# Kernel tuning notes

Hardware: AMD Instinct MI355X
Metric: run time of the kernel (lower is better)

The kernel has to match this reference:

```python
import jax, jax.numpy as jnp
import numpy as np

BLOCK = 16
NUM_HEADS = 12
EMBED = 768
LN_EPS = 1e-6


def setup_inputs() -> dict:
    key = jax.random.key(0)
    ks = jax.random.split(key, 6)
    H = W = 1024
    x = jax.random.normal(ks[0], (H, W), dtype=jnp.float32)
    # Conv2d(1, EMBED, kernel=BLOCK, stride=BLOCK) weights, flattened to [E, b*b]
    proj_w = jax.random.normal(ks[1], (EMBED, BLOCK * BLOCK), dtype=jnp.float32) * 0.02
    proj_b = jax.random.normal(ks[2], (EMBED,), dtype=jnp.float32) * 0.02
    ln_g = jnp.ones((EMBED,), dtype=jnp.float32)
    ln_b = jnp.zeros((EMBED,), dtype=jnp.float32)
    # nn.Linear(E, 3E, bias=False): weight [3E, E]
    qkv_w = jax.random.normal(ks[3], (3 * EMBED, EMBED), dtype=jnp.float32) * 0.02
    return {"x": x, "proj_w": proj_w, "proj_b": proj_b,
            "ln_g": ln_g, "ln_b": ln_b, "qkv_w": qkv_w}


def reference(x, proj_w, proj_b, ln_g, ln_b, qkv_w):
    H, W = x.shape
    b = BLOCK
    # Patch embed: conv with kernel=stride=b on a single-channel image is
    # exactly patchify + matmul. Token order matches flatten(2) (row-major).
    patches = x.reshape(H // b, b, W // b, b).transpose(0, 2, 1, 3)
    patches = patches.reshape((H // b) * (W // b), b * b)      # [N, b*b]
    tok = patches @ proj_w.T + proj_b                          # [N, E]

    # LayerNorm (eps=1e-6)
    mu = jnp.mean(tok, axis=-1, keepdims=True)
    var = jnp.mean(jnp.square(tok - mu), axis=-1, keepdims=True)
    tok = (tok - mu) * jax.lax.rsqrt(var + LN_EPS) * ln_g + ln_b

    # Attention (batch = 1)
    N, C = tok.shape
    h, d = NUM_HEADS, C // NUM_HEADS
    qkv = (tok @ qkv_w.T).reshape(N, 3, h, d)                  # [N, 3, h, d]
    q = qkv[:, 0].transpose(1, 0, 2)                            # [h, N, d]
    k = qkv[:, 1].transpose(1, 0, 2)
    v = qkv[:, 2].transpose(1, 0, 2)
    scale = d ** -0.5
    attn = jax.nn.softmax(jnp.einsum('hnd,hmd->hnm', q, k) * scale, axis=-1)
    out = jnp.einsum('hnm,hmd->hnd', attn, v)                   # [h, N, d]
    out = out.transpose(1, 0, 2).reshape(N, C)                  # [N, C]
    return out[None]                                            # [1, N, C]
```

## Files before the change

kernel.cpp:

```cpp
#include <hip/hip_runtime.h>
#include <hip/hip_bf16.h>

typedef __bf16 bf16_t;
typedef __attribute__((ext_vector_type(8))) __bf16 bf16x8;
typedef __attribute__((ext_vector_type(4))) __bf16 bf16x4;
typedef __attribute__((ext_vector_type(4))) float f32x4;
typedef __attribute__((ext_vector_type(4))) unsigned int uint4v;

#define QSCALE 0.1803368801111204f

static __device__ inline void glds16(const bf16_t* g, bf16_t* l) {
    __builtin_amdgcn_global_load_lds(
        (__attribute__((address_space(1))) const void*)g,
        (__attribute__((address_space(3))) void*)l,
        16, 0, 0);
}

static __device__ inline float hwexp2(float x) {
#if __has_builtin(__builtin_amdgcn_exp2f)
    return __builtin_amdgcn_exp2f(x);
#else
    float r;
    asm("v_exp_f32 %0, %1" : "=v"(r) : "v"(x));
    return r;
#endif
}

static __device__ inline unsigned int pack_trunc(float lo, float hi) {
    return __builtin_amdgcn_perm(__builtin_bit_cast(unsigned int, hi),
                                 __builtin_bit_cast(unsigned int, lo),
                                 0x07060302u);
}

__global__ void cvt2_kernel(const float* __restrict__ a, bf16_t* __restrict__ oa, int na4,
                            const float* __restrict__ b, bf16_t* __restrict__ ob, int nb4) {
    int i = blockIdx.x * 256 + threadIdx.x;
    if (i < na4) {
        float4 v = ((const float4*)a)[i];
        bf16x4 o = {(bf16_t)v.x, (bf16_t)v.y, (bf16_t)v.z, (bf16_t)v.w};
        ((bf16x4*)oa)[i] = o;
    } else {
        int j = i - na4;
        if (j < nb4) {
            float4 v = ((const float4*)b)[j];
            bf16x4 o = {(bf16_t)v.x, (bf16_t)v.y, (bf16_t)v.z, (bf16_t)v.w};
            ((bf16x4*)ob)[j] = o;
        }
    }
}

__global__ __launch_bounds__(256) void patch_gemm(const float* __restrict__ x,
                                                  const bf16_t* __restrict__ pw,
                                                  const float* __restrict__ pb,
                                                  float* __restrict__ tok) {
    const int bm = blockIdx.x;
    const int bn = blockIdx.y;
    const int tid = threadIdx.x;

    __shared__ bf16_t At[64][264];
    __shared__ bf16_t Bt[64][264];

    #pragma unroll
    for (int t = 0; t < 16; t++) {
        int linear = tid + t * 256;
        int ml = linear >> 6;
        int kv = (linear & 63) << 2;
        int n = bm * 64 + ml;
        int pr = n >> 6, pc = n & 63;
        int i = kv >> 4, j = kv & 15;
        float4 v = *(const float4*)(x + (pr * 16 + i) * 1024 + pc * 16 + j);
        bf16x4 o = {(bf16_t)v.x, (bf16_t)v.y, (bf16_t)v.z, (bf16_t)v.w};
        *(bf16x4*)(&At[ml][kv]) = o;
    }
    #pragma unroll
    for (int t = 0; t < 8; t++) {
        int linear = tid + t * 256;
        int nl = linear >> 5;
        int kv = (linear & 31) << 3;
        *(int4*)(&Bt[nl][kv]) = *(const int4*)(pw + (size_t)(bn * 64 + nl) * 256 + kv);
    }
    __syncthreads();

    const int lane = tid & 63, wid = tid >> 6, ln = lane & 15, quad = lane >> 4;
    f32x4 acc[4];
    #pragma unroll
    for (int s = 0; s < 4; s++) acc[s] = {0.f, 0.f, 0.f, 0.f};

    #pragma unroll
    for (int kk = 0; kk < 8; kk++) {
        bf16x8 af = *(const bf16x8*)(&At[wid * 16 + ln][kk * 32 + quad * 8]);
        #pragma unroll
        for (int s = 0; s < 4; s++) {
            bf16x8 bfr = *(const bf16x8*)(&Bt[s * 16 + ln][kk * 32 + quad * 8]);
            acc[s] = __builtin_amdgcn_mfma_f32_16x16x32_bf16(af, bfr, acc[s], 0, 0, 0);
        }
    }

    #pragma unroll
    for (int s = 0; s < 4; s++) {
        int e = bn * 64 + s * 16 + ln;
        float bias = pb[e];
        #pragma unroll
        for (int r = 0; r < 4; r++) {
            int m = bm * 64 + wid * 16 + quad * 4 + r;
            tok[(size_t)m * 768 + e] = acc[s][r] + bias;
        }
    }
}

__global__ __launch_bounds__(256) void ln_kernel(const float* __restrict__ tok,
                                                 const float* __restrict__ g,
                                                 const float* __restrict__ b,
                                                 bf16_t* __restrict__ out) {
    const int n = blockIdx.x;
    const int tid = threadIdx.x;
    const float* row = tok + (size_t)n * 768;
    float x0 = row[tid], x1 = row[tid + 256], x2 = row[tid + 512];
    float s = x0 + x1 + x2;
    float s2 = x0 * x0 + x1 * x1 + x2 * x2;
    #pragma unroll
    for (int off = 32; off; off >>= 1) {
        s += __shfl_xor(s, off);
        s2 += __shfl_xor(s2, off);
    }
    __shared__ float ws1[4], ws2[4];
    int wid = tid >> 6;
    if ((tid & 63) == 0) { ws1[wid] = s; ws2[wid] = s2; }
    __syncthreads();
    s = ws1[0] + ws1[1] + ws1[2] + ws1[3];
    s2 = ws2[0] + ws2[1] + ws2[2] + ws2[3];
    float mu = s * (1.f / 768.f);
    float var = s2 * (1.f / 768.f) - mu * mu;
    float r = rsqrtf(var + 1e-6f);
    bf16_t* orow = out + (size_t)n * 768;
    orow[tid]       = (bf16_t)((x0 - mu) * r * g[tid]       + b[tid]);
    orow[tid + 256] = (bf16_t)((x1 - mu) * r * g[tid + 256] + b[tid + 256]);
    orow[tid + 512] = (bf16_t)((x2 - mu) * r * g[tid + 512] + b[tid + 512]);
}

__global__ __launch_bounds__(256) void qkv_gemm(const bf16_t* __restrict__ tokb,
                                                const bf16_t* __restrict__ wq,
                                                bf16_t* __restrict__ qb,
                                                bf16_t* __restrict__ kswz,
                                                bf16_t* __restrict__ vswz) {
    const int bm = blockIdx.x;
    const int bn = blockIdx.y;
    const int tid = threadIdx.x;
    const int wid = tid >> 6, lane = tid & 63;
    const int ln = lane & 15, quad = lane >> 4;
    const int wm = wid & 1, wn = wid >> 1;

    __shared__ bf16_t At[128 * 64];
    __shared__ bf16_t Bt[128 * 64];

    f32x4 acc[4][4];
    #pragma unroll
    for (int sm = 0; sm < 4; sm++)
        #pragma unroll
        for (int sn = 0; sn < 4; sn++) acc[sm][sn] = {0.f, 0.f, 0.f, 0.f};

    const int srow = wid * 32 + (lane >> 3);
    const int scol = (lane & 7) * 8;

    for (int kb0 = 0; kb0 < 768; kb0 += 64) {
        __syncthreads();
        #pragma unroll
        for (int i = 0; i < 4; i++) {
            glds16(tokb + (size_t)(bm * 128 + srow + i * 8) * 768 + kb0 + scol,
                   At + wid * 2048 + i * 512);
            glds16(wq + (size_t)(bn * 128 + srow + i * 8) * 768 + kb0 + scol,
                   Bt + wid * 2048 + i * 512);
        }
        __syncthreads();
        #pragma unroll
        for (int kk = 0; kk < 2; kk++) {
            bf16x8 af[4], bfr[4];
            #pragma unroll
            for (int s = 0; s < 4; s++) {
                af[s]  = *(const bf16x8*)(At + (wm * 64 + s * 16 + ln) * 64 + kk * 32 + quad * 8);
                bfr[s] = *(const bf16x8*)(Bt + (wn * 64 + s * 16 + ln) * 64 + kk * 32 + quad * 8);
            }
            #pragma unroll
            for (int sm = 0; sm < 4; sm++)
                #pragma unroll
                for (int sn = 0; sn < 4; sn++)
                    acc[sm][sn] = __builtin_amdgcn_mfma_f32_16x16x32_bf16(af[sm], bfr[sn], acc[sm][sn], 0, 0, 0);
        }
    }

    const int sidx = bn / 6;
    const int head = (bn % 6) * 2 + wn;
    #pragma unroll
    for (int sn = 0; sn < 4; sn++) {
        int dc = sn * 16 + ln;
        #pragma unroll
        for (int sm = 0; sm < 4; sm++) {
            #pragma unroll
            for (int r = 0; r < 4; r++) {
                int m = bm * 128 + wm * 64 + sm * 16 + quad * 4 + r;
                float v = acc[sm][sn][r];
                if (sidx == 0) {
                    qb[((size_t)(head * 4096 + m)) * 64 + dc] = (bf16_t)(v * QSCALE);
                } else if (sidx == 1) {
                    bf16_t val = (bf16_t)v;
                    int kt = m >> 6, sb = (m >> 4) & 3, lnk = m & 15;
                    int half = dc >> 5, quadk = (dc >> 3) & 3, j = dc & 7;
                    int l = quadk * 16 + lnk;
                    kswz[((size_t)(head * 64 + kt)) * 4096 + sb * 1024 + half * 512 + l * 8 + j] = val;
                } else {
                    bf16_t val = (bf16_t)v;
                    int kt = m >> 6, keyl = m & 63;
                    int sblk = keyl >> 4;
                    int mm = sblk >> 1, tb = sblk & 1;
                    int w16 = keyl & 15, qv = w16 >> 2, jj = w16 & 3;
                    int jp = tb * 4 + jj;
                    int db = dc >> 4, lnv = dc & 15;
                    int l = qv * 16 + lnv;
                    vswz[((size_t)(head * 64 + kt)) * 4096 + ((mm * 4 + db) * 64 + l) * 8 + jp] = val;
                }
            }
        }
    }
}

__global__ __launch_bounds__(256, 2) void attn_partial(const bf16_t* __restrict__ qbuf,
                                                       const bf16_t* __restrict__ kswz,
                                                       const bf16_t* __restrict__ vswz,
                                                       float* __restrict__ raw0,
                                                       float* __restrict__ raw1,
                                                       float* __restrict__ l_part) {
    const int h = blockIdx.y;
    const int chunk = blockIdx.z;
    const int tid = threadIdx.x;
    const int wid = tid >> 6;
    const int lane = tid & 63;
    const int ln = lane & 15, quad = lane >> 4;
    const int q0 = blockIdx.x * 128;

    __shared__ bf16_t Kf[2][4096];
    __shared__ bf16_t Vf[2][4096];

    bf16x8 qf[2][2];
    #pragma unroll
    for (int g = 0; g < 2; g++) {
        const int q0g = q0 + wid * 32 + g * 16;
        const bf16_t* qrow = qbuf + ((size_t)h * 4096 + q0g + ln) * 64;
        qf[g][0] = *(const bf16x8*)(qrow + quad * 8);
        qf[g][1] = *(const bf16x8*)(qrow + 32 + quad * 8);
    }

    bf16x8 ones;
    #pragma unroll
    for (int i = 0; i < 8; i++) ones[i] = (bf16_t)1.0f;

    const bf16_t* kg = kswz + (size_t)h * 64 * 4096 + (size_t)chunk * 32 * 4096;
    const bf16_t* vg = vswz + (size_t)h * 64 * 4096 + (size_t)chunk * 32 * 4096;

    f32x4 accO[2][4];
    f32x4 accL[2];
    #pragma unroll
    for (int g = 0; g < 2; g++) {
        accL[g] = {0.f, 0.f, 0.f, 0.f};
        #pragma unroll
        for (int d = 0; d < 4; d++) accO[g][d] = {0.f, 0.f, 0.f, 0.f};
    }

    auto stage = [&](int tile, int buf) {
        const bf16_t* kt_g = kg + (size_t)tile * 4096;
        const bf16_t* vt_g = vg + (size_t)tile * 4096;
        #pragma unroll
        for (int i = 0; i < 2; i++) {
            glds16(kt_g + wid * 1024 + i * 512 + lane * 8, &Kf[buf][wid * 1024 + i * 512]);
            glds16(vt_g + wid * 1024 + i * 512 + lane * 8, &Vf[buf][wid * 1024 + i * 512]);
        }
    };

    auto compute = [&](const bf16_t* Kb, const bf16_t* Vb) {
        #pragma unroll
        for (int m = 0; m < 2; m++) {
            bf16x8 vf[4];
            #pragma unroll
            for (int db = 0; db < 4; db++)
                vf[db] = *(const bf16x8*)(Vb + m * 2048 + db * 512 + lane * 8);
            bf16x8 kfa0 = *(const bf16x8*)(Kb + (2 * m) * 1024 + lane * 8);
            bf16x8 kfa1 = *(const bf16x8*)(Kb + (2 * m) * 1024 + 512 + lane * 8);
            bf16x8 kfb0 = *(const bf16x8*)(Kb + (2 * m + 1) * 1024 + lane * 8);
            bf16x8 kfb1 = *(const bf16x8*)(Kb + (2 * m + 1) * 1024 + 512 + lane * 8);
            #pragma unroll
            for (int g = 0; g < 2; g++) {
                f32x4 z = {0.f, 0.f, 0.f, 0.f};
                f32x4 SA = __builtin_amdgcn_mfma_f32_16x16x32_bf16(kfa0, qf[g][0], z, 0, 0, 0);
                SA = __builtin_amdgcn_mfma_f32_16x16x32_bf16(kfa1, qf[g][1], SA, 0, 0, 0);
                f32x4 SB = __builtin_amdgcn_mfma_f32_16x16x32_bf16(kfb0, qf[g][0], z, 0, 0, 0);
                SB = __builtin_amdgcn_mfma_f32_16x16x32_bf16(kfb1, qf[g][1], SB, 0, 0, 0);

                float e0 = hwexp2(SA[0]), e1 = hwexp2(SA[1]), e2 = hwexp2(SA[2]), e3 = hwexp2(SA[3]);
                float e4 = hwexp2(SB[0]), e5 = hwexp2(SB[1]), e6 = hwexp2(SB[2]), e7 = hwexp2(SB[3]);
                uint4v u = {pack_trunc(e0, e1), pack_trunc(e2, e3),
                            pack_trunc(e4, e5), pack_trunc(e6, e7)};
                bf16x8 pb = __builtin_bit_cast(bf16x8, u);
                accL[g] = __builtin_amdgcn_mfma_f32_16x16x32_bf16(ones, pb, accL[g], 0, 0, 0);
                #pragma unroll
                for (int db = 0; db < 4; db++)
                    accO[g][db] = __builtin_amdgcn_mfma_f32_16x16x32_bf16(vf[db], pb, accO[g][db], 0, 0, 0);
            }
        }
    };

    stage(0, 0);

    for (int kt = 0; kt < 32; kt += 2) {
        __builtin_amdgcn_s_barrier();
        stage(kt + 1, 1);
        __builtin_amdgcn_s_waitcnt(0x0F74);
        __builtin_amdgcn_s_barrier();
        compute(&Kf[0][0], &Vf[0][0]);
        __builtin_amdgcn_s_barrier();
        if (kt + 2 < 32) {
            stage(kt + 2, 0);
            __builtin_amdgcn_s_waitcnt(0x0F74);
        } else {
            __builtin_amdgcn_s_waitcnt(0x0F70);
        }
        __builtin_amdgcn_s_barrier();
        compute(&Kf[1][0], &Vf[1][0]);
    }

    float* base = chunk ? raw1 : raw0;
    #pragma unroll
    for (int g = 0; g < 2; g++) {
        const int qg = q0 + wid * 32 + g * 16 + ln;
        if (quad == 0) l_part[(size_t)chunk * 49152 + h * 4096 + qg] = accL[g][0];
        float* op = base + (size_t)qg * 768 + h * 64 + quad * 4;
        #pragma unroll
        for (int db = 0; db < 4; db++)
            *(f32x4*)(op + db * 16) = accO[g][db];
    }
}

__global__ __launch_bounds__(256) void norm_kernel(const float* __restrict__ raw0,
                                                   const float* __restrict__ raw1,
                                                   const float* __restrict__ l_part,
                                                   float* __restrict__ out) {
    const int q = blockIdx.x;
    const int tid = threadIdx.x;
    __shared__ float linv[12];
    if (tid < 12)
        linv[tid] = 1.0f / (l_part[tid * 4096 + q] + l_part[49152 + tid * 4096 + q]);
    __syncthreads();
    #pragma unroll
    for (int t = 0; t < 3; t++) {
        int c = tid + t * 256;
        size_t idx = (size_t)q * 768 + c;
        out[idx] = (raw0[idx] + raw1[idx]) * linv[c >> 6];
    }
}

extern "C" void kernel_launch(void* const* d_in, const int* in_sizes, int n_in,
                              void* d_out, int out_size, void* d_ws, size_t ws_size,
                              hipStream_t stream) {
    const float* x      = (const float*)d_in[0];
    const float* proj_w = (const float*)d_in[1];
    const float* proj_b = (const float*)d_in[2];
    const float* ln_g   = (const float*)d_in[3];
    const float* ln_b   = (const float*)d_in[4];
    const float* qkv_w  = (const float*)d_in[5];
    float* out = (float*)d_out;

    char* ws = (char*)d_ws;
    float*  tok_pre = (float*)(ws + 0);
    bf16_t* tok_b   = (bf16_t*)(ws + 12582912);
    bf16_t* pw_b    = (bf16_t*)(ws + 18874368);
    bf16_t* qw_b    = (bf16_t*)(ws + 19267584);
    bf16_t* qbuf    = (bf16_t*)(ws + 22806528);
    bf16_t* kswz    = (bf16_t*)(ws + 29097984);
    bf16_t* vswz    = (bf16_t*)(ws + 35389440);
    float*  raw0    = tok_pre;
    float*  raw1    = out;
    float*  l_part  = (float*)pw_b;

    cvt2_kernel<<<1920, 256, 0, stream>>>(proj_w, pw_b, 49152, qkv_w, qw_b, 442368);
    patch_gemm<<<dim3(64, 12), 256, 0, stream>>>(x, pw_b, proj_b, tok_pre);
    ln_kernel<<<4096, 256, 0, stream>>>(tok_pre, ln_g, ln_b, tok_b);
    qkv_gemm<<<dim3(32, 18), 256, 0, stream>>>(tok_b, qw_b, qbuf, kswz, vswz);
    attn_partial<<<dim3(32, 12, 2), 256, 0, stream>>>(qbuf, kswz, vswz, raw0, raw1, l_part);
    norm_kernel<<<4096, 256, 0, stream>>>(raw0, raw1, l_part, out);
}
```

Baseline: 189.1 us.

## Double-buffer QKV GEMM LDS loads with XOR swizzle and narrower N tile

The QKV projection GEMM now stages its tiles into two LDS buffers, so the next K slice is fetched while the current one is consumed, using explicit vmcnt waits and barriers. Columns are XOR-swizzled in LDS to avoid bank conflicts on the fragment reads. The N tile shrinks from 128 to 64, which doubles the grid to 1152 blocks and maps one block to one head. The aim is to hide global-load latency and improve occupancy in a kernel that is a small part of the total. The trade-off is more reuse of B per block lost and added synchronisation complexity.

```diff
diff --git a/kernel.cpp b/kernel.cpp
--- a/kernel.cpp
+++ b/kernel.cpp
@@ -150,49 +150,81 @@
     const int ln = lane & 15, quad = lane >> 4;
     const int wm = wid & 1, wn = wid >> 1;
 
-    __shared__ bf16_t At[128 * 64];
-    __shared__ bf16_t Bt[128 * 64];
-
-    f32x4 acc[4][4];
+    __shared__ bf16_t Asw[2][8192];
+    __shared__ bf16_t Bsw[2][4096];
+
+    f32x4 acc[4][2];
     #pragma unroll
     for (int sm = 0; sm < 4; sm++)
         #pragma unroll
-        for (int sn = 0; sn < 4; sn++) acc[sm][sn] = {0.f, 0.f, 0.f, 0.f};
-
-    const int srow = wid * 32 + (lane >> 3);
-    const int scol = (lane & 7) * 8;
-
-    for (int kb0 = 0; kb0 < 768; kb0 += 64) {
-        __syncthreads();
+        for (int sn = 0; sn < 2; sn++) acc[sm][sn] = {0.f, 0.f, 0.f, 0.f};
+
+    auto stage = [&](int kb0, int buf) {
         #pragma unroll
         for (int i = 0; i < 4; i++) {
-            glds16(tokb + (size_t)(bm * 128 + srow + i * 8) * 768 + kb0 + scol,
-                   At + wid * 2048 + i * 512);
-            glds16(wq + (size_t)(bn * 128 + srow + i * 8) * 768 + kb0 + scol,
-                   Bt + wid * 2048 + i * 512);
-        }
-        __syncthreads();
+            int L = wid * 256 + i * 64 + lane;
+            int r = L >> 3, c = L & 7;
+            int gc = c ^ (r & 7);
+            glds16(tokb + (size_t)(bm * 128 + r) * 768 + kb0 + gc * 8,
+                   Asw[buf] + (wid * 256 + i * 64) * 8);
+        }
+        #pragma unroll
+        for (int i = 0; i < 2; i++) {
+            int L = wid * 128 + i * 64 + lane;
+            int r = L >> 3, c = L & 7;
+            int gc = c ^ (r & 7);
+            glds16(wq + (size_t)(bn * 64 + r) * 768 + kb0 + gc * 8,
+                   Bsw[buf] + (wid * 128 + i * 64) * 8);
+        }
+    };
+
+    auto compute = [&](const bf16_t* Ab, const bf16_t* Bb) {
         #pragma unroll
         for (int kk = 0; kk < 2; kk++) {
-            bf16x8 af[4], bfr[4];
-            #pragma unroll
-            for (int s = 0; s < 4; s++) {
-                af[s]  = *(const bf16x8*)(At + (wm * 64 + s * 16 + ln) * 64 + kk * 32 + quad * 8);
-                bfr[s] = *(const bf16x8*)(Bt + (wn * 64 + s * 16 + ln) * 64 + kk * 32 + quad * 8);
+            const int c = (kk * 4 + quad) ^ (ln & 7);
+            bf16x8 af[4], bfr[2];
+            #pragma unroll
+            for (int sm = 0; sm < 4; sm++) {
+                int row = wm * 64 + sm * 16 + ln;
+                af[sm] = *(const bf16x8*)(Ab + (row * 8 + c) * 8);
+            }
+            #pragma unroll
+            for (int sn = 0; sn < 2; sn++) {
+                int row = wn * 32 + sn * 16 + ln;
+                bfr[sn] = *(const bf16x8*)(Bb + (row * 8 + c) * 8);
             }
             #pragma unroll
             for (int sm = 0; sm < 4; sm++)
                 #pragma unroll
-                for (int sn = 0; sn < 4; sn++)
+                for (int sn = 0; sn < 2; sn++)
                     acc[sm][sn] = __builtin_amdgcn_mfma_f32_16x16x32_bf16(af[sm], bfr[sn], acc[sm][sn], 0, 0, 0);
         }
-    }
-
-    const int sidx = bn / 6;
-    const int head = (bn % 6) * 2 + wn;
-    #pragma unroll
-    for (int sn = 0; sn < 4; sn++) {
-        int dc = sn * 16 + ln;
+    };
+
+    stage(0, 0);
+
+    for (int s = 0; s < 12; s += 2) {
+        __builtin_amdgcn_s_barrier();
+        stage((s + 1) * 64, 1);
+        __builtin_amdgcn_s_waitcnt(0x0F76);
+        __builtin_amdgcn_s_barrier();
+        compute(Asw[0], Bsw[0]);
+        __builtin_amdgcn_s_barrier();
+        if (s + 2 < 12) {
+            stage((s + 2) * 64, 0);
+            __builtin_amdgcn_s_waitcnt(0x0F76);
+        } else {
+            __builtin_amdgcn_s_waitcnt(0x0F70);
+        }
+        __builtin_amdgcn_s_barrier();
+        compute(Asw[1], Bsw[1]);
+    }
+
+    const int sidx = bn / 12;
+    const int head = bn % 12;
+    #pragma unroll
+    for (int sn = 0; sn < 2; sn++) {
+        int dc = wn * 32 + sn * 16 + ln;
         #pragma unroll
         for (int sm = 0; sm < 4; sm++) {
             #pragma unroll
@@ -382,7 +414,7 @@
     cvt2_kernel<<<1920, 256, 0, stream>>>(proj_w, pw_b, 49152, qkv_w, qw_b, 442368);
     patch_gemm<<<dim3(64, 12), 256, 0, stream>>>(x, pw_b, proj_b, tok_pre);
     ln_kernel<<<4096, 256, 0, stream>>>(tok_pre, ln_g, ln_b, tok_b);
-    qkv_gemm<<<dim3(32, 18), 256, 0, stream>>>(tok_b, qw_b, qbuf, kswz, vswz);
+    qkv_gemm<<<dim3(32, 36), 256, 0, stream>>>(tok_b, qw_b, qbuf, kswz, vswz);
     attn_partial<<<dim3(32, 12, 2), 256, 0, stream>>>(qbuf, kswz, vswz, raw0, raw1, l_part);
     norm_kernel<<<4096, 256, 0, stream>>>(raw0, raw1, l_part, out);
 }
```

New measurement: 179.0 us. -5.4%, faster.
